# Kernel tuning notes

Hardware: AMD Instinct MI355X
Metric: run time of the kernel (lower is better)

## Reference

```python
import jax, jax.numpy as jnp
import numpy as np

L, H, NH, V, T, B, K = 12, 768, 12, 30522, 512, 4, 21
DH = H // NH
INV_SQRT_DH = 1.0 / float(np.sqrt(DH))
NEG = -1e4  # BERT additive mask value
LN_EPS = 1e-12


def _ln(x, g, b):
    m = x.mean(-1, keepdims=True)
    v = jnp.var(x, axis=-1, keepdims=True)
    return (x - m) * jax.lax.rsqrt(v + LN_EPS) * g + b


def _encoder(input_ids, attention_mask, word_emb, pos_emb, tok_emb, emb_g, emb_b,
             Wqkv, bqkv, Wo, bo, ln1_g, ln1_b, W1, b1, W2, b2, ln2_g, ln2_b):
    Bv, Tv = input_ids.shape
    h = word_emb[input_ids] + pos_emb[None, :Tv] + tok_emb[0]  # token_type_ids = 0
    h = _ln(h, emb_g, emb_b)
    bias = (1.0 - attention_mask[:, None, None, :].astype(h.dtype)) * NEG  # [B,1,1,T]

    def layer(h, xs):
        wqkv, bq, wo, bo_, g1, b1_, w1, bb1, w2, bb2, g2, b2_ = xs
        qkv = h @ wqkv + bq  # [B,T,3H]
        q, k, v = jnp.split(qkv, 3, axis=-1)
        def hd(x):
            return x.reshape(Bv, Tv, NH, DH).transpose(0, 2, 1, 3)
        q, k, v = hd(q), hd(k), hd(v)
        scores = jnp.einsum('bhqd,bhkd->bhqk', q, k) * INV_SQRT_DH + bias
        ctx = jnp.einsum('bhqk,bhkd->bhqd', jax.nn.softmax(scores, axis=-1), v)
        ctx = ctx.transpose(0, 2, 1, 3).reshape(Bv, Tv, H)
        h = _ln(h + ctx @ wo + bo_, g1, b1_)  # post-LN (BERT)
        ff = jax.nn.gelu(h @ w1 + bb1, approximate=False) @ w2 + bb2
        h = _ln(h + ff, g2, b2_)
        return h, None

    h, _ = jax.lax.scan(layer, h, (Wqkv, bqkv, Wo, bo, ln1_g, ln1_b, W1, b1, W2, b2, ln2_g, ln2_b))
    return h


def _crf_nll(emissions, tags, mask, start, end, trans):
    # emissions [B,T,K], tags [B,T] int, mask [B,T] bool; torchcrf reduction='mean'
    Bv, Tv, Kv = emissions.shape
    maskf = mask.astype(emissions.dtype)
    # numerator: score of the gold path
    num = start[tags[:, 0]] + emissions[jnp.arange(Bv), 0, tags[:, 0]]
    em_t = jnp.take_along_axis(emissions, tags[..., None], axis=-1)[..., 0]  # [B,T]
    tr_t = trans[tags[:, :-1], tags[:, 1:]]  # [B,T-1]
    num = num + jnp.sum((tr_t + em_t[:, 1:]) * maskf[:, 1:], axis=1)
    last_idx = mask.sum(axis=1).astype(jnp.int32) - 1
    last_tag = jnp.take_along_axis(tags, last_idx[:, None], axis=1)[:, 0]
    num = num + end[last_tag]
    # denominator: forward algorithm (logsumexp recursion over time)
    alpha0 = start[None, :] + emissions[:, 0]  # [B,K]

    def step(alpha, xs):
        em, m = xs  # em [B,K], m [B] bool
        nxt = jax.scipy.special.logsumexp(alpha[:, :, None] + trans[None] + em[:, None, :], axis=1)
        return jnp.where(m[:, None], nxt, alpha), None

    alpha, _ = jax.lax.scan(step, alpha0, (emissions[:, 1:].transpose(1, 0, 2), mask[:, 1:].T))
    den = jax.scipy.special.logsumexp(alpha + end[None, :], axis=1)
    return -(num - den).mean()


def _viterbi(emissions, mask, start, end, trans):
    # Returns [B,T] int32 best paths; padded tail repeats the last valid tag.
    Bv, Tv, Kv = emissions.shape
    score0 = start[None, :] + emissions[:, 0]
    ident = jnp.broadcast_to(jnp.arange(Kv), (Bv, Kv))

    def step(score, xs):
        em, m = xs
        cand = score[:, :, None] + trans[None]  # [B,K_prev,K_next]
        idx = jnp.where(m[:, None], jnp.argmax(cand, axis=1), ident)
        nxt = jnp.max(cand, axis=1) + em
        return jnp.where(m[:, None], nxt, score), idx

    score, hist = jax.lax.scan(step, score0, (emissions[:, 1:].transpose(1, 0, 2), mask[:, 1:].T))
    last = jnp.argmax(score + end[None, :], axis=1)  # [B]

    def back(nxt_tag, idx):
        prev = jnp.take_along_axis(idx, nxt_tag[:, None], axis=1)[:, 0]
        return prev, nxt_tag

    tag0, rest = jax.lax.scan(back, last, hist, reverse=True)  # rest[i] = tag at t=i+1
    return jnp.concatenate([tag0[None], rest], axis=0).T.astype(jnp.int32)


def setup_inputs():
    key = jax.random.key(0)
    ks = jax.random.split(key, 16)
    s = 0.02

    def n(k, shape):
        return (s * jax.random.normal(k, shape)).astype(jnp.float32)

    def u(k, shape):
        return jax.random.uniform(k, shape, minval=-0.1, maxval=0.1).astype(jnp.float32)

    p = {}
    p['input_ids'] = jax.random.randint(ks[0], (B, T), 0, V)
    lengths = jax.random.randint(ks[1], (B,), T // 2, T + 1)
    p['attention_mask'] = (jnp.arange(T)[None, :] < lengths[:, None]).astype(jnp.int32)
    p['valid_mask'] = p['attention_mask']
    p['labels'] = jax.random.randint(ks[2], (B, T), 0, K)
    p['word_emb'] = n(ks[3], (V, H))
    p['pos_emb'] = n(ks[4], (T, H))
    p['tok_emb'] = n(ks[5], (2, H))
    p['emb_g'] = jnp.ones((H,), jnp.float32)
    p['emb_b'] = jnp.zeros((H,), jnp.float32)
    p['Wqkv'] = n(ks[6], (L, H, 3 * H))
    p['bqkv'] = jnp.zeros((L, 3 * H), jnp.float32)
    p['Wo'] = n(ks[7], (L, H, H))
    p['bo'] = jnp.zeros((L, H), jnp.float32)
    p['ln1_g'] = jnp.ones((L, H), jnp.float32)
    p['ln1_b'] = jnp.zeros((L, H), jnp.float32)
    p['W1'] = n(ks[8], (L, H, 4 * H))
    p['b1'] = jnp.zeros((L, 4 * H), jnp.float32)
    p['W2'] = n(ks[9], (L, 4 * H, H))
    p['b2'] = jnp.zeros((L, H), jnp.float32)
    p['ln2_g'] = jnp.ones((L, H), jnp.float32)
    p['ln2_b'] = jnp.zeros((L, H), jnp.float32)
    p['Wc'] = n(ks[10], (H, K))
    p['bc'] = jnp.zeros((K,), jnp.float32)
    p['crf_start'] = u(ks[11], (K,))
    p['crf_end'] = u(ks[12], (K,))
    p['crf_trans'] = u(ks[13], (K, K))
    return p


def reference(input_ids, attention_mask, valid_mask, labels,
              word_emb, pos_emb, tok_emb, emb_g, emb_b,
              Wqkv, bqkv, Wo, bo, ln1_g, ln1_b, W1, b1, W2, b2, ln2_g, ln2_b,
              Wc, bc, crf_start, crf_end, crf_trans):
    h = _encoder(input_ids, attention_mask, word_emb, pos_emb, tok_emb, emb_g, emb_b,
                 Wqkv, bqkv, Wo, bo, ln1_g, ln1_b, W1, b1, W2, b2, ln2_g, ln2_b)
    emissions = h @ Wc + bc  # dropout is identity in eval/reference mode
    mask = attention_mask.astype(bool)
    nll = _crf_nll(emissions, labels, mask, crf_start, crf_end, crf_trans)
    decoded = _viterbi(emissions, mask, crf_start, crf_end, crf_trans)
    return nll, decoded
```

## Files before the change

kernel.cpp:

```cpp
#include <hip/hip_runtime.h>
#include <math.h>

constexpr int NLAYER = 12;
constexpr int H = 768;
constexpr int NH = 12;
constexpr int DH = 64;
constexpr int T = 512;
constexpr int B = 4;
constexpr int K = 21;
constexpr int BT = B * T;
constexpr float NEGB = -10000.0f;
constexpr float LNEPS = 1e-12f;
constexpr float INV_SQRT_DH = 0.125f;

typedef __attribute__((ext_vector_type(8))) short bf16x8;
typedef __attribute__((ext_vector_type(4))) float f32x4;
typedef __attribute__((ext_vector_type(4))) unsigned short u16x4;

#define WAIT_VMCNT(n) asm volatile("s_waitcnt vmcnt(" #n ")")

__device__ __forceinline__ float wave_sum_f(float v) {
#pragma unroll
  for (int off = 32; off > 0; off >>= 1) v += __shfl_xor(v, off);
  return v;
}
__device__ __forceinline__ int wave_sum_i(int v) {
#pragma unroll
  for (int off = 32; off > 0; off >>= 1) v += __shfl_xor(v, off);
  return v;
}
__device__ __forceinline__ float readlane_f(float v, int i) {
  return __uint_as_float(__builtin_amdgcn_readlane(__float_as_uint(v), i));
}
__device__ __forceinline__ unsigned short f32_bf16_rn(float x) {
  unsigned int u = __float_as_uint(x);
  u += 0x7fffu + ((u >> 16) & 1u);
  return (unsigned short)(u >> 16);
}
__device__ __forceinline__ void split_bf16(float x, unsigned short& h, unsigned short& l) {
  h = f32_bf16_rn(x);
  float hf = __uint_as_float((unsigned int)h << 16);
  l = f32_bf16_rn(x - hf);
}
__device__ __forceinline__ void block_reduce_sum2(float& s, float& q) {
  __shared__ float red[8];
  s = wave_sum_f(s);
  q = wave_sum_f(q);
  int lane = threadIdx.x & 63, wid = threadIdx.x >> 6;
  if (lane == 0) { red[wid] = s; red[4 + wid] = q; }
  __syncthreads();
  s = red[0] + red[1] + red[2] + red[3];
  q = red[4] + red[5] + red[6] + red[7];
}

__global__ __launch_bounds__(256) void embed_ln_kernel(
    const int* __restrict__ ids, const float* __restrict__ wemb,
    const float* __restrict__ pemb, const float* __restrict__ temb,
    const float* __restrict__ g, const float* __restrict__ bta,
    float* __restrict__ h, unsigned short* __restrict__ hh,
    unsigned short* __restrict__ hl) {
  int row = blockIdx.x;
  int t = row % T;
  int id = ids[row];
  const float* wp = wemb + (size_t)id * H;
  const float* pp = pemb + (size_t)t * H;
  float x[3];
  float s = 0.f, q = 0.f;
#pragma unroll
  for (int i = 0; i < 3; i++) {
    int c = threadIdx.x + i * 256;
    x[i] = wp[c] + pp[c] + temb[c];
    s += x[i];
    q += x[i] * x[i];
  }
  block_reduce_sum2(s, q);
  float mean = s * (1.0f / H);
  float var = q * (1.0f / H) - mean * mean;
  float inv = rsqrtf(var + LNEPS);
#pragma unroll
  for (int i = 0; i < 3; i++) {
    int c = threadIdx.x + i * 256;
    float y = (x[i] - mean) * inv * g[c] + bta[c];
    h[(size_t)row * H + c] = y;
    unsigned short yh, yl;
    split_bf16(y, yh, yl);
    hh[(size_t)row * H + c] = yh;
    hl[(size_t)row * H + c] = yl;
  }
}

__global__ __launch_bounds__(256) void add_ln_kernel(
    float* __restrict__ h, const float* __restrict__ add,
    const float* __restrict__ g, const float* __restrict__ bta,
    unsigned short* __restrict__ hh, unsigned short* __restrict__ hl) {
  int row = blockIdx.x;
  size_t base = (size_t)row * H;
  float x[3];
  float s = 0.f, q = 0.f;
#pragma unroll
  for (int i = 0; i < 3; i++) {
    int c = threadIdx.x + i * 256;
    x[i] = h[base + c] + add[base + c];
    s += x[i];
    q += x[i] * x[i];
  }
  block_reduce_sum2(s, q);
  float mean = s * (1.0f / H);
  float var = q * (1.0f / H) - mean * mean;
  float inv = rsqrtf(var + LNEPS);
#pragma unroll
  for (int i = 0; i < 3; i++) {
    int c = threadIdx.x + i * 256;
    float y = (x[i] - mean) * inv * g[c] + bta[c];
    h[base + c] = y;
    unsigned short yh, yl;
    split_bf16(y, yh, yl);
    hh[base + c] = yh;
    hl[base + c] = yl;
  }
}

__global__ __launch_bounds__(256) void wconv_kernel(
    const float* __restrict__ w0, const float* __restrict__ w1,
    const float* __restrict__ w2, const float* __restrict__ w3,
    unsigned short* __restrict__ Wth, unsigned short* __restrict__ Wtl) {
  __shared__ float tile[32][33];
  int bid = blockIdx.x;
  const float* src;
  int Kd, N, tk, tn;
  size_t off;
  if (bid < 1728) {
    src = w0; Kd = 768; N = 2304; tk = bid / 72; tn = bid % 72; off = 0;
  } else if (bid < 2304) {
    int t2 = bid - 1728; src = w1; Kd = 768; N = 768; tk = t2 / 24; tn = t2 % 24;
    off = 1769472;
  } else if (bid < 4608) {
    int t2 = bid - 2304; src = w2; Kd = 768; N = 3072; tk = t2 / 96; tn = t2 % 96;
    off = 2359296;
  } else {
    int t2 = bid - 4608; src = w3; Kd = 3072; N = 768; tk = t2 / 24; tn = t2 % 24;
    off = 4718592;
  }
  int tid = threadIdx.x;
  int k0 = tk * 32, n0 = tn * 32;
  int r = tid >> 3, c = (tid & 7) * 4;
  float4 v = *(const float4*)(src + (size_t)(k0 + r) * N + n0 + c);
  tile[r][c + 0] = v.x; tile[r][c + 1] = v.y; tile[r][c + 2] = v.z; tile[r][c + 3] = v.w;
  __syncthreads();
  u16x4 hv, lv;
#pragma unroll
  for (int q2 = 0; q2 < 4; q2++) {
    unsigned short sh, sl;
    split_bf16(tile[c + q2][r], sh, sl);
    hv[q2] = sh; lv[q2] = sl;
  }
  size_t dst = off + (size_t)(n0 + r) * Kd + k0 + c;
  *(u16x4*)(Wth + dst) = hv;
  *(u16x4*)(Wtl + dst) = lv;
}

template <int OUTMODE>
__global__ __launch_bounds__(256) void gemm_bf3_kernel(
    const unsigned short* __restrict__ Ah, const unsigned short* __restrict__ Al,
    const unsigned short* __restrict__ Wth, const unsigned short* __restrict__ Wtl,
    const float* __restrict__ bias, float* __restrict__ C,
    unsigned short* __restrict__ Ch, unsigned short* __restrict__ Cl,
    unsigned short* __restrict__ Kh, unsigned short* __restrict__ Kl,
    unsigned short* __restrict__ Vth, unsigned short* __restrict__ Vtl,
    int N, int Kd, int ncols) {
  constexpr int AW = 64 * 32;
  constexpr int WW = 128 * 32;
  constexpr int DBS = 2 * AW + 2 * WW;
  __shared__ short lds_s[2 * DBS];
  int tid = threadIdx.x;
  int lane = tid & 63, wid = tid >> 6;
  int wr = wid >> 1, wc = wid & 1;
  int tiles = gridDim.x;
  int q8 = tiles >> 3;
  int wg = (blockIdx.x & 7) * q8 + (blockIdx.x >> 3);
  int bm = (wg / ncols) * 64, bn = (wg % ncols) * 128;

  f32x4 acc[2][4] = {};
  int lrow = lane >> 2;
  int lslot_sw = (lane & 3) ^ ((lrow >> 1) & 3);

  const unsigned short* sbase;
  int rowbase, ldsoff, nchunks;
  if (wid == 0)      { sbase = Ah;  rowbase = bm; ldsoff = 0;            nchunks = 4; }
  else if (wid == 1) { sbase = Al;  rowbase = bm; ldsoff = AW;           nchunks = 4; }
  else if (wid == 2) { sbase = Wth; rowbase = bn; ldsoff = 2 * AW;       nchunks = 8; }
  else               { sbase = Wtl; rowbase = bn; ldsoff = 2 * AW + WW;  nchunks = 8; }

  const unsigned short* srcbase = sbase + (size_t)(rowbase + lrow) * Kd + lslot_sw * 8;

  auto STAGE = [&](int db, int k0) {
#pragma unroll
    for (int c = 0; c < 8; c++) {
      if (c < nchunks) {
        const unsigned short* src = srcbase + (size_t)(c * 16) * Kd + k0;
        char* dst = ((char*)lds_s) + (db * DBS + ldsoff) * 2 + c * 1024 + lane * 16;
        __builtin_amdgcn_global_load_lds(
            (const __attribute__((address_space(1))) void*)src,
            (__attribute__((address_space(3))) void*)dst, 16, 0, 0);
      }
    }
  };

  const int NT = Kd / 32;
  STAGE(0, 0);
  for (int kt = 0; kt < NT; kt++) {
    int cur = kt & 1;
    bool more = (kt + 1 < NT);
    if (more) STAGE(cur ^ 1, (kt + 1) * 32);
    if (more) {
      if (wid < 2) { WAIT_VMCNT(4); } else { WAIT_VMCNT(8); }
    } else {
      WAIT_VMCNT(0);
    }
    __builtin_amdgcn_s_barrier();
    __builtin_amdgcn_sched_barrier(0);

    int lr = lane & 15, lg = lane >> 4;
    int slot = (lg ^ ((lr >> 1) & 3)) * 8;
    int cb = cur * DBS;
    bf16x8 af_h[2], af_l[2], wf_h[4], wf_l[4];
#pragma unroll
    for (int i = 0; i < 2; i++) {
      int e = (wr * 32 + i * 16 + lr) * 32 + slot;
      af_h[i] = *(const bf16x8*)&lds_s[cb + e];
      af_l[i] = *(const bf16x8*)&lds_s[cb + AW + e];
    }
#pragma unroll
    for (int j = 0; j < 4; j++) {
      int e = (wc * 64 + j * 16 + lr) * 32 + slot;
      wf_h[j] = *(const bf16x8*)&lds_s[cb + 2 * AW + e];
      wf_l[j] = *(const bf16x8*)&lds_s[cb + 2 * AW + WW + e];
    }
#pragma unroll
    for (int i = 0; i < 2; i++)
#pragma unroll
      for (int j = 0; j < 4; j++) {
        acc[i][j] = __builtin_amdgcn_mfma_f32_16x16x32_bf16(af_h[i], wf_h[j], acc[i][j], 0, 0, 0);
        acc[i][j] = __builtin_amdgcn_mfma_f32_16x16x32_bf16(af_l[i], wf_h[j], acc[i][j], 0, 0, 0);
        acc[i][j] = __builtin_amdgcn_mfma_f32_16x16x32_bf16(af_h[i], wf_l[j], acc[i][j], 0, 0, 0);
      }
    asm volatile("s_waitcnt lgkmcnt(0)");
    __builtin_amdgcn_sched_barrier(0);
    __builtin_amdgcn_s_barrier();
    __builtin_amdgcn_sched_barrier(0);
  }

  int lr = lane & 15, lg = lane >> 4;
#pragma unroll
  for (int i = 0; i < 2; i++) {
#pragma unroll
    for (int j = 0; j < 4; j++) {
      int row = bm + wr * 32 + i * 16 + lg * 4;
      int col = bn + wc * 64 + j * 16 + lr;
      float bv = bias[col];
      if (OUTMODE == 2) {
        int sec = col / 768;
        int within = col % 768;
        int hidx = within >> 6, d = within & 63;
        int b = row >> 9, t = row & 511;
        int bh = b * NH + hidx;
        if (sec == 2) {
          u16x4 hv, lv;
#pragma unroll
          for (int r = 0; r < 4; r++) {
            unsigned short sh, sl;
            split_bf16(acc[i][j][r] + bv, sh, sl);
            hv[r] = sh; lv[r] = sl;
          }
          size_t idx = ((size_t)bh * 64 + d) * T + t;
          *(u16x4*)(Vth + idx) = hv;
          *(u16x4*)(Vtl + idx) = lv;
        } else {
          unsigned short* dh = (sec == 0) ? Ch : Kh;
          unsigned short* dl = (sec == 0) ? Cl : Kl;
#pragma unroll
          for (int r = 0; r < 4; r++) {
            unsigned short sh, sl;
            split_bf16(acc[i][j][r] + bv, sh, sl);
            size_t idx = ((size_t)bh * T + t + r) * 64 + d;
            dh[idx] = sh;
            dl[idx] = sl;
          }
        }
      } else {
#pragma unroll
        for (int r = 0; r < 4; r++) {
          float v = acc[i][j][r] + bv;
          if (OUTMODE == 1) {
            v = 0.5f * v * (1.0f + erff(v * 0.70710678118654752f));
            unsigned short sh, sl;
            split_bf16(v, sh, sl);
            Ch[(size_t)(row + r) * N + col] = sh;
            Cl[(size_t)(row + r) * N + col] = sl;
          } else {
            C[(size_t)(row + r) * N + col] = v;
          }
        }
      }
    }
  }
}

__global__ __launch_bounds__(256) void attn_kernel(
    const unsigned short* __restrict__ qh, const unsigned short* __restrict__ ql,
    const unsigned short* __restrict__ kh, const unsigned short* __restrict__ kl,
    const unsigned short* __restrict__ vth, const unsigned short* __restrict__ vtl,
    const int* __restrict__ mask,
    unsigned short* __restrict__ cth, unsigned short* __restrict__ ctl) {
  int id = blockIdx.x;
  int bh = (id & 7) * 6 + ((id >> 3) % 6);
  int i0 = (id / 48) * 64;
  int b = bh / NH, hidx = bh % NH;
  int tid = threadIdx.x, lane = tid & 63, w = tid >> 6;
  int lr = lane & 15, lg = lane >> 4;
  __shared__ float bias_s[T];
  __shared__ short p_h[4][16 * 64];
  __shared__ short p_l[4][16 * 64];
  for (int i = tid; i < T; i += 256)
    bias_s[i] = (1.0f - (float)mask[b * T + i]) * NEGB;
  __syncthreads();

  const unsigned short* qb_h = qh + ((size_t)bh * T + i0 + w * 16 + lr) * 64 + lg * 8;
  const unsigned short* qb_l = ql + ((size_t)bh * T + i0 + w * 16 + lr) * 64 + lg * 8;
  bf16x8 qf_h0 = *(const bf16x8*)qb_h;
  bf16x8 qf_h1 = *(const bf16x8*)(qb_h + 32);
  bf16x8 qf_l0 = *(const bf16x8*)qb_l;
  bf16x8 qf_l1 = *(const bf16x8*)(qb_l + 32);

  float m_run[4], l_run[4];
#pragma unroll
  for (int r = 0; r < 4; r++) { m_run[r] = -3.0e38f; l_run[r] = 0.f; }
  f32x4 acc_o[4] = {};

  for (int kt = 0; kt < T / 64; kt++) {
    f32x4 s[4] = {};
#pragma unroll
    for (int jf = 0; jf < 4; jf++) {
      size_t kb = ((size_t)bh * T + kt * 64 + jf * 16 + lr) * 64 + lg * 8;
      bf16x8 kf_h0 = *(const bf16x8*)(kh + kb);
      bf16x8 kf_h1 = *(const bf16x8*)(kh + kb + 32);
      bf16x8 kf_l0 = *(const bf16x8*)(kl + kb);
      bf16x8 kf_l1 = *(const bf16x8*)(kl + kb + 32);
      s[jf] = __builtin_amdgcn_mfma_f32_16x16x32_bf16(qf_h0, kf_h0, s[jf], 0, 0, 0);
      s[jf] = __builtin_amdgcn_mfma_f32_16x16x32_bf16(qf_h1, kf_h1, s[jf], 0, 0, 0);
      s[jf] = __builtin_amdgcn_mfma_f32_16x16x32_bf16(qf_l0, kf_h0, s[jf], 0, 0, 0);
      s[jf] = __builtin_amdgcn_mfma_f32_16x16x32_bf16(qf_l1, kf_h1, s[jf], 0, 0, 0);
      s[jf] = __builtin_amdgcn_mfma_f32_16x16x32_bf16(qf_h0, kf_l0, s[jf], 0, 0, 0);
      s[jf] = __builtin_amdgcn_mfma_f32_16x16x32_bf16(qf_h1, kf_l1, s[jf], 0, 0, 0);
    }
    float mt[4] = {-3.0e38f, -3.0e38f, -3.0e38f, -3.0e38f};
#pragma unroll
    for (int jf = 0; jf < 4; jf++) {
      float bcol = bias_s[kt * 64 + jf * 16 + lr];
#pragma unroll
      for (int r = 0; r < 4; r++) {
        float v = s[jf][r] * INV_SQRT_DH + bcol;
        s[jf][r] = v;
        mt[r] = fmaxf(mt[r], v);
      }
    }
#pragma unroll
    for (int r = 0; r < 4; r++) {
      mt[r] = fmaxf(mt[r], __shfl_xor(mt[r], 1));
      mt[r] = fmaxf(mt[r], __shfl_xor(mt[r], 2));
      mt[r] = fmaxf(mt[r], __shfl_xor(mt[r], 4));
      mt[r] = fmaxf(mt[r], __shfl_xor(mt[r], 8));
    }
#pragma unroll
    for (int r = 0; r < 4; r++) {
      float mn = fmaxf(m_run[r], mt[r]);
      float sc = __expf(m_run[r] - mn);
      m_run[r] = mn;
      l_run[r] *= sc;
#pragma unroll
      for (int jf = 0; jf < 4; jf++) acc_o[jf][r] *= sc;
    }
    float ps[4] = {0.f, 0.f, 0.f, 0.f};
#pragma unroll
    for (int jf = 0; jf < 4; jf++) {
#pragma unroll
      for (int r = 0; r < 4; r++) {
        float p = __expf(s[jf][r] - m_run[r]);
        ps[r] += p;
        unsigned short sh, sl;
        split_bf16(p, sh, sl);
        int q = lg * 4 + r;
        int col = jf * 16 + lr;
        int addr = q * 64 + (((col >> 3) ^ (q & 7)) << 3) + (col & 7);
        p_h[w][addr] = sh;
        p_l[w][addr] = sl;
      }
    }
#pragma unroll
    for (int r = 0; r < 4; r++) {
      ps[r] += __shfl_xor(ps[r], 1);
      ps[r] += __shfl_xor(ps[r], 2);
      ps[r] += __shfl_xor(ps[r], 4);
      ps[r] += __shfl_xor(ps[r], 8);
      l_run[r] += ps[r];
    }
#pragma unroll
    for (int c = 0; c < 2; c++) {
      int aaddr = lr * 64 + (((4 * c + lg) ^ (lr & 7)) << 3);
      bf16x8 pa_h = *(const bf16x8*)&p_h[w][aaddr];
      bf16x8 pa_l = *(const bf16x8*)&p_l[w][aaddr];
#pragma unroll
      for (int jf = 0; jf < 4; jf++) {
        size_t vb = ((size_t)bh * 64 + jf * 16 + lr) * T + kt * 64 + c * 32 + lg * 8;
        bf16x8 vf_h = *(const bf16x8*)(vth + vb);
        bf16x8 vf_l = *(const bf16x8*)(vtl + vb);
        acc_o[jf] = __builtin_amdgcn_mfma_f32_16x16x32_bf16(pa_h, vf_h, acc_o[jf], 0, 0, 0);
        acc_o[jf] = __builtin_amdgcn_mfma_f32_16x16x32_bf16(pa_l, vf_h, acc_o[jf], 0, 0, 0);
        acc_o[jf] = __builtin_amdgcn_mfma_f32_16x16x32_bf16(pa_h, vf_l, acc_o[jf], 0, 0, 0);
      }
    }
  }
  float inv[4];
#pragma unroll
  for (int r = 0; r < 4; r++) inv[r] = 1.0f / l_run[r];
#pragma unroll
  for (int jf = 0; jf < 4; jf++) {
#pragma unroll
    for (int r = 0; r < 4; r++) {
      float v = acc_o[jf][r] * inv[r];
      unsigned short sh, sl;
      split_bf16(v, sh, sl);
      size_t idx = ((size_t)(b * T) + i0 + w * 16 + lg * 4 + r) * H + hidx * 64 + jf * 16 + lr;
      cth[idx] = sh;
      ctl[idx] = sl;
    }
  }
}

__global__ __launch_bounds__(256) void wct_kernel(
    const float* __restrict__ Wc, float* __restrict__ WcT) {
  int id = blockIdx.x * 256 + threadIdx.x;
  int k = id / H, d = id % H;
  WcT[id] = Wc[d * K + k];
}

__global__ __launch_bounds__(256) void classifier_kernel(
    const float* __restrict__ h, const float* __restrict__ WcT,
    const float* __restrict__ bc, float* __restrict__ em) {
  int id = blockIdx.x * 256 + threadIdx.x;
  if (id >= BT * K) return;
  int row = id / K, k = id % K;
  const float4* h4 = (const float4*)(h + (size_t)row * H);
  const float4* w4 = (const float4*)(WcT + (size_t)k * H);
  float acc = bc[k];
  for (int d = 0; d < H / 4; d++) {
    float4 a = h4[d], b = w4[d];
    acc = fmaf(a.x, b.x, acc);
    acc = fmaf(a.y, b.y, acc);
    acc = fmaf(a.z, b.z, acc);
    acc = fmaf(a.w, b.w, acc);
  }
  em[id] = acc;
}

#define MRG(vo, io, va, ia, vb, ib) \
  float vo = ((vb) > (va)) ? (vb) : (va); \
  int io = ((vb) > (va)) ? (ib) : (ia);

__global__ __launch_bounds__(64) void crf_fused_kernel(
    const float* __restrict__ em, const int* __restrict__ labels,
    const int* __restrict__ mask, const float* __restrict__ start,
    const float* __restrict__ endv, const float* __restrict__ trans,
    float* __restrict__ parts, float* __restrict__ outdec) {
  __shared__ float em_s[T * K];
  __shared__ int mask_s[T];
  __shared__ unsigned char hist_s[(T - 1) * K];
  __shared__ float sc_s[32];
  int b = blockIdx.x & 3;
  int role = blockIdx.x >> 2;
  int j = threadIdx.x;
  const float* eb = em + (size_t)b * T * K;
  for (int i = j; i < T * K / 4; i += 64)
    ((float4*)em_s)[i] = ((const float4*)eb)[i];
  for (int i = j; i < T; i += 64) mask_s[i] = mask[b * T + i];
  __syncthreads();
  bool act = (j < K);
  float tr[K];
#pragma unroll
  for (int i = 0; i < K; i++) tr[i] = act ? trans[i * K + j] : 0.f;

  int cntloc = 0;
  for (int t = j; t < T; t += 64) cntloc += mask_s[t];
  int cnt = wave_sum_i(cntloc);

  if (role == 0) {
    const int* tb = labels + b * T;
    float numloc = 0.f;
    for (int t = j; t < T; t += 64) {
      if (t >= 1 && mask_s[t]) {
        int tp = tb[t - 1], tc = tb[t];
        numloc += trans[tp * K + tc] + em_s[t * K + tc];
      }
    }
    float num = wave_sum_f(numloc);
    float etr[K];
#pragma unroll
    for (int i = 0; i < K; i++) etr[i] = __expf(tr[i]);
    float alpha = act ? (start[j] + em_s[j]) : 0.f;
    float emv = act ? em_s[K + j] : 0.f;
    for (int t = 1; t < cnt; t++) {
      float emv_n = (act && (t + 1) < cnt) ? em_s[(t + 1) * K + j] : 0.f;
      float m0 = readlane_f(alpha, 0);
      float ee = __expf(alpha - m0);
      float e0 = readlane_f(ee, 0),  e1 = readlane_f(ee, 1),  e2 = readlane_f(ee, 2);
      float e3 = readlane_f(ee, 3),  e4 = readlane_f(ee, 4),  e5 = readlane_f(ee, 5);
      float e6 = readlane_f(ee, 6),  e7 = readlane_f(ee, 7),  e8 = readlane_f(ee, 8);
      float e9 = readlane_f(ee, 9),  e10 = readlane_f(ee, 10), e11 = readlane_f(ee, 11);
      float e12 = readlane_f(ee, 12), e13 = readlane_f(ee, 13), e14 = readlane_f(ee, 14);
      float e15 = readlane_f(ee, 15), e16 = readlane_f(ee, 16), e17 = readlane_f(ee, 17);
      float e18 = readlane_f(ee, 18), e19 = readlane_f(ee, 19), e20 = readlane_f(ee, 20);
      float a0 = fmaf(e16, etr[16], fmaf(e12, etr[12], fmaf(e8, etr[8],  fmaf(e4, etr[4], e0 * etr[0]))));
      float a1 = fmaf(e17, etr[17], fmaf(e13, etr[13], fmaf(e9, etr[9],  fmaf(e5, etr[5], e1 * etr[1]))));
      float a2 = fmaf(e18, etr[18], fmaf(e14, etr[14], fmaf(e10, etr[10], fmaf(e6, etr[6], e2 * etr[2]))));
      float a3 = fmaf(e19, etr[19], fmaf(e15, etr[15], fmaf(e11, etr[11], fmaf(e7, etr[7], e3 * etr[3]))));
      float ssum = fmaf(e20, etr[20], (a0 + a1) + (a2 + a3));
      float nxt = __logf(ssum) + m0 + emv;
      if (act) alpha = nxt;
      emv = emv_n;
    }
    float aj = act ? (alpha + endv[j]) : -3.0e38f;
    float mm = aj;
#pragma unroll
    for (int off = 32; off > 0; off >>= 1) mm = fmaxf(mm, __shfl_xor(mm, off));
    float e2v = act ? __expf(aj - mm) : 0.f;
    float s2 = wave_sum_f(e2v);
    float den = __logf(s2) + mm;
    if (j == 0) {
      int tag0 = tb[0];
      float numtot = num + start[tag0] + em_s[tag0] + endv[tb[cnt - 1]];
      parts[b] = numtot - den;
    }
  } else {
    float score = act ? (start[j] + em_s[j]) : 0.f;
    float emv = act ? em_s[K + j] : 0.f;
    for (int t = 1; t < cnt; t++) {
      float emv_n = (act && (t + 1) < cnt) ? em_s[(t + 1) * K + j] : 0.f;
      float c0 = readlane_f(score, 0) + tr[0],   c1 = readlane_f(score, 1) + tr[1];
      float c2 = readlane_f(score, 2) + tr[2],   c3 = readlane_f(score, 3) + tr[3];
      float c4 = readlane_f(score, 4) + tr[4],   c5 = readlane_f(score, 5) + tr[5];
      float c6 = readlane_f(score, 6) + tr[6],   c7 = readlane_f(score, 7) + tr[7];
      float c8 = readlane_f(score, 8) + tr[8],   c9 = readlane_f(score, 9) + tr[9];
      float c10 = readlane_f(score, 10) + tr[10], c11 = readlane_f(score, 11) + tr[11];
      float c12 = readlane_f(score, 12) + tr[12], c13 = readlane_f(score, 13) + tr[13];
      float c14 = readlane_f(score, 14) + tr[14], c15 = readlane_f(score, 15) + tr[15];
      float c16 = readlane_f(score, 16) + tr[16], c17 = readlane_f(score, 17) + tr[17];
      float c18 = readlane_f(score, 18) + tr[18], c19 = readlane_f(score, 19) + tr[19];
      float c20 = readlane_f(score, 20) + tr[20];
      MRG(m0v, m0i, c0, 0, c1, 1)
      MRG(m1v, m1i, c2, 2, c3, 3)
      MRG(m2v, m2i, c4, 4, c5, 5)
      MRG(m3v, m3i, c6, 6, c7, 7)
      MRG(m4v, m4i, c8, 8, c9, 9)
      MRG(m5v, m5i, c10, 10, c11, 11)
      MRG(m6v, m6i, c12, 12, c13, 13)
      MRG(m7v, m7i, c14, 14, c15, 15)
      MRG(m8v, m8i, c16, 16, c17, 17)
      MRG(m9v, m9i, c18, 18, c19, 19)
      MRG(p0v, p0i, m0v, m0i, m1v, m1i)
      MRG(p1v, p1i, m2v, m2i, m3v, m3i)
      MRG(p2v, p2i, m4v, m4i, m5v, m5i)
      MRG(p3v, p3i, m6v, m6i, m7v, m7i)
      MRG(p4v, p4i, m8v, m8i, m9v, m9i)
      MRG(r0v, r0i, p0v, p0i, p1v, p1i)
      MRG(r1v, r1i, p2v, p2i, p3v, p3i)
      MRG(r2v, r2i, p4v, p4i, c20, 20)
      MRG(s0v, s0i, r0v, r0i, r1v, r1i)
      MRG(fv, fi, s0v, s0i, r2v, r2i)
      if (act) {
        hist_s[(t - 1) * K + j] = (unsigned char)fi;
        score = fv + emv;
      }
      emv = emv_n;
    }
    if (act) sc_s[j] = score + endv[j];
    __syncthreads();
    if (j == 0) {
      float best = -3.0e38f;
      int last = 0;
#pragma unroll
      for (int i = 0; i < K; i++)
        if (sc_s[i] > best) { best = sc_s[i]; last = i; }
      for (int t = cnt - 1; t < T; t++) outdec[b * T + t] = (float)last;
      int cur = last;
      for (int t = cnt - 1; t >= 1; t--) {
        cur = hist_s[(t - 1) * K + cur];
        outdec[b * T + (t - 1)] = (float)cur;
      }
    }
  }
}

__global__ void nll_final_kernel(const float* __restrict__ parts,
                                 float* __restrict__ out) {
  out[0] = -0.25f * (parts[0] + parts[1] + parts[2] + parts[3]);
}

extern "C" void kernel_launch(void* const* d_in, const int* in_sizes, int n_in,
                              void* d_out, int out_size, void* d_ws, size_t ws_size,
                              hipStream_t stream) {
  (void)in_sizes; (void)n_in; (void)out_size; (void)ws_size;
  const int* ids    = (const int*)d_in[0];
  const int* amask  = (const int*)d_in[1];
  const int* labels = (const int*)d_in[3];
  const float* wemb = (const float*)d_in[4];
  const float* pemb = (const float*)d_in[5];
  const float* temb = (const float*)d_in[6];
  const float* eg   = (const float*)d_in[7];
  const float* ebta = (const float*)d_in[8];
  const float* Wqkv = (const float*)d_in[9];
  const float* bqkv = (const float*)d_in[10];
  const float* Wo   = (const float*)d_in[11];
  const float* bo   = (const float*)d_in[12];
  const float* ln1g = (const float*)d_in[13];
  const float* ln1b = (const float*)d_in[14];
  const float* W1   = (const float*)d_in[15];
  const float* b1   = (const float*)d_in[16];
  const float* W2   = (const float*)d_in[17];
  const float* b2   = (const float*)d_in[18];
  const float* ln2g = (const float*)d_in[19];
  const float* ln2b = (const float*)d_in[20];
  const float* Wc   = (const float*)d_in[21];
  const float* bc   = (const float*)d_in[22];
  const float* cst  = (const float*)d_in[23];
  const float* cen  = (const float*)d_in[24];
  const float* ctr  = (const float*)d_in[25];
  float* out = (float*)d_out;

  float* ws = (float*)d_ws;
  float* fp = ws;
  float* h = fp;                 fp += 1572864;
  unsigned short* hh  = (unsigned short*)fp; fp += 786432;
  unsigned short* hl  = (unsigned short*)fp; fp += 786432;
  unsigned short* qhp = (unsigned short*)fp; fp += 786432;
  unsigned short* qlp = (unsigned short*)fp; fp += 786432;
  unsigned short* khp = (unsigned short*)fp; fp += 786432;
  unsigned short* klp = (unsigned short*)fp; fp += 786432;
  unsigned short* vtp = (unsigned short*)fp; fp += 786432;
  unsigned short* vlp = (unsigned short*)fp; fp += 786432;
  unsigned short* cth = (unsigned short*)fp; fp += 786432;
  unsigned short* ctl = (unsigned short*)fp; fp += 786432;
  float* tmp = fp;               fp += 1572864;
  unsigned short* gh  = (unsigned short*)fp; fp += 3145728;
  unsigned short* gl  = (unsigned short*)fp; fp += 3145728;
  unsigned short* Wth = (unsigned short*)fp; fp += 3538944;
  unsigned short* Wtl = (unsigned short*)fp; fp += 3538944;
  float* em = fp;                fp += 43008;
  float* parts = fp;             fp += 8;
  float* WcT = fp;               fp += 16128;

  embed_ln_kernel<<<BT, 256, 0, stream>>>(ids, wemb, pemb, temb, eg, ebta, h, hh, hl);
  wct_kernel<<<63, 256, 0, stream>>>(Wc, WcT);

  for (int l = 0; l < NLAYER; l++) {
    const float* bqkv_l = bqkv + (size_t)l * 3 * H;
    const float* bo_l   = bo + (size_t)l * H;
    const float* b1_l   = b1 + (size_t)l * 4 * H;
    const float* b2_l   = b2 + (size_t)l * H;

    wconv_kernel<<<6912, 256, 0, stream>>>(
        Wqkv + (size_t)l * H * 3 * H, Wo + (size_t)l * H * H,
        W1 + (size_t)l * H * 4 * H, W2 + (size_t)l * 4 * H * H, Wth, Wtl);

    gemm_bf3_kernel<2><<<576, 256, 0, stream>>>(
        hh, hl, Wth, Wtl, bqkv_l, nullptr, qhp, qlp, khp, klp,
        vtp, vlp, 3 * H, H, 18);
    attn_kernel<<<384, 256, 0, stream>>>(
        qhp, qlp, khp, klp, vtp, vlp, amask, cth, ctl);
    gemm_bf3_kernel<0><<<192, 256, 0, stream>>>(
        cth, ctl, Wth + 1769472, Wtl + 1769472, bo_l, tmp,
        nullptr, nullptr, nullptr, nullptr, nullptr, nullptr, H, H, 6);
    add_ln_kernel<<<BT, 256, 0, stream>>>(h, tmp, ln1g + (size_t)l * H, ln1b + (size_t)l * H, hh, hl);
    gemm_bf3_kernel<1><<<768, 256, 0, stream>>>(
        hh, hl, Wth + 2359296, Wtl + 2359296, b1_l, nullptr, gh, gl,
        nullptr, nullptr, nullptr, nullptr, 4 * H, H, 24);
    gemm_bf3_kernel<0><<<192, 256, 0, stream>>>(
        gh, gl, Wth + 4718592, Wtl + 4718592, b2_l, tmp,
        nullptr, nullptr, nullptr, nullptr, nullptr, nullptr, H, 4 * H, 6);
    add_ln_kernel<<<BT, 256, 0, stream>>>(h, tmp, ln2g + (size_t)l * H, ln2b + (size_t)l * H, hh, hl);
  }

  classifier_kernel<<<(BT * K + 255) / 256, 256, 0, stream>>>(h, WcT, bc, em);
  crf_fused_kernel<<<8, 64, 0, stream>>>(em, labels, amask, cst, cen, ctr, parts, out + 1);
  nll_final_kernel<<<1, 1, 0, stream>>>(parts, out);
}
```

Measured before the change: 3.153 ms.

## Overlap next-layer weight conversion with attention; load GEMM operands directly into registers

Weight split/transpose for layer l+1 is now fused into the attention launch as extra blocks, writing into a double-buffered weight area so conversion overlaps attention instead of running as its own serial kernel. Layer 0 weights are converted once up front. The GEMM also drops its LDS double-buffered staging and instead loads MFMA fragments straight from global memory into registers, with a two-stage register ping-pong. This removes LDS traffic and barriers but gives up cross-wave operand sharing through LDS, relies on L1/L2 for reuse, and increases register pressure.

```diff
diff --git a/kernel.cpp b/kernel.cpp
--- a/kernel.cpp
+++ b/kernel.cpp
@@ -17,7 +17,7 @@
 typedef __attribute__((ext_vector_type(4))) float f32x4;
 typedef __attribute__((ext_vector_type(4))) unsigned short u16x4;
 
-#define WAIT_VMCNT(n) asm volatile("s_waitcnt vmcnt(" #n ")")
+constexpr size_t WL_SHORTS = 7077888;
 
 __device__ __forceinline__ float wave_sum_f(float v) {
 #pragma unroll
@@ -120,12 +120,11 @@
   }
 }
 
-__global__ __launch_bounds__(256) void wconv_kernel(
-    const float* __restrict__ w0, const float* __restrict__ w1,
+__device__ __forceinline__ void wconv_body(
+    int bid, int tid, const float* __restrict__ w0, const float* __restrict__ w1,
     const float* __restrict__ w2, const float* __restrict__ w3,
-    unsigned short* __restrict__ Wth, unsigned short* __restrict__ Wtl) {
-  __shared__ float tile[32][33];
-  int bid = blockIdx.x;
+    unsigned short* __restrict__ Wth, unsigned short* __restrict__ Wtl,
+    float (*tile)[33]) {
   const float* src;
   int Kd, N, tk, tn;
   size_t off;
@@ -141,7 +140,6 @@
     int t2 = bid - 4608; src = w3; Kd = 3072; N = 768; tk = t2 / 24; tn = t2 % 24;
     off = 4718592;
   }
-  int tid = threadIdx.x;
   int k0 = tk * 32, n0 = tn * 32;
   int r = tid >> 3, c = (tid & 7) * 4;
   float4 v = *(const float4*)(src + (size_t)(k0 + r) * N + n0 + c);
@@ -159,8 +157,42 @@
   *(u16x4*)(Wtl + dst) = lv;
 }
 
+__global__ __launch_bounds__(256) void wconv_kernel(
+    const float* __restrict__ w0, const float* __restrict__ w1,
+    const float* __restrict__ w2, const float* __restrict__ w3,
+    unsigned short* __restrict__ Wth, unsigned short* __restrict__ Wtl) {
+  __shared__ float tile[32][33];
+  wconv_body(blockIdx.x, threadIdx.x, w0, w1, w2, w3, Wth, Wtl, tile);
+}
+
+#define MFMA3(AI, AJ, AH, AL, WH, WL)                                              \
+  acc[AI][AJ] = __builtin_amdgcn_mfma_f32_16x16x32_bf16(AH, WH, acc[AI][AJ], 0, 0, 0); \
+  acc[AI][AJ] = __builtin_amdgcn_mfma_f32_16x16x32_bf16(AL, WH, acc[AI][AJ], 0, 0, 0); \
+  acc[AI][AJ] = __builtin_amdgcn_mfma_f32_16x16x32_bf16(AH, WL, acc[AI][AJ], 0, 0, 0);
+
+#define DECLS(S) bf16x8 a0h##S, a1h##S, a0l##S, a1l##S,                 \
+      w0h##S, w1h##S, w2h##S, w3h##S, w0l##S, w1l##S, w2l##S, w3l##S
+
+#define LOADS(S, KT) do { int ko = (KT) * 32;                            \
+    a0h##S = *(const bf16x8*)(aH0 + ko); a1h##S = *(const bf16x8*)(aH1 + ko); \
+    a0l##S = *(const bf16x8*)(aL0 + ko); a1l##S = *(const bf16x8*)(aL1 + ko); \
+    w0h##S = *(const bf16x8*)(wH0 + ko); w1h##S = *(const bf16x8*)(wH1 + ko); \
+    w2h##S = *(const bf16x8*)(wH2 + ko); w3h##S = *(const bf16x8*)(wH3 + ko); \
+    w0l##S = *(const bf16x8*)(wL0 + ko); w1l##S = *(const bf16x8*)(wL1 + ko); \
+    w2l##S = *(const bf16x8*)(wL2 + ko); w3l##S = *(const bf16x8*)(wL3 + ko); } while (0)
+
+#define MFMAS(S)                                        \
+  MFMA3(0, 0, a0h##S, a0l##S, w0h##S, w0l##S)           \
+  MFMA3(0, 1, a0h##S, a0l##S, w1h##S, w1l##S)           \
+  MFMA3(0, 2, a0h##S, a0l##S, w2h##S, w2l##S)           \
+  MFMA3(0, 3, a0h##S, a0l##S, w3h##S, w3l##S)           \
+  MFMA3(1, 0, a1h##S, a1l##S, w0h##S, w0l##S)           \
+  MFMA3(1, 1, a1h##S, a1l##S, w1h##S, w1l##S)           \
+  MFMA3(1, 2, a1h##S, a1l##S, w2h##S, w2l##S)           \
+  MFMA3(1, 3, a1h##S, a1l##S, w3h##S, w3l##S)
+
 template <int OUTMODE>
-__global__ __launch_bounds__(256) void gemm_bf3_kernel(
+__global__ __launch_bounds__(256) void gemm_reg_kernel(
     const unsigned short* __restrict__ Ah, const unsigned short* __restrict__ Al,
     const unsigned short* __restrict__ Wth, const unsigned short* __restrict__ Wtl,
     const float* __restrict__ bias, float* __restrict__ C,
@@ -168,10 +200,6 @@
     unsigned short* __restrict__ Kh, unsigned short* __restrict__ Kl,
     unsigned short* __restrict__ Vth, unsigned short* __restrict__ Vtl,
     int N, int Kd, int ncols) {
-  constexpr int AW = 64 * 32;
-  constexpr int WW = 128 * 32;
-  constexpr int DBS = 2 * AW + 2 * WW;
-  __shared__ short lds_s[2 * DBS];
   int tid = threadIdx.x;
   int lane = tid & 63, wid = tid >> 6;
   int wr = wid >> 1, wc = wid & 1;
@@ -179,78 +207,33 @@
   int q8 = tiles >> 3;
   int wg = (blockIdx.x & 7) * q8 + (blockIdx.x >> 3);
   int bm = (wg / ncols) * 64, bn = (wg % ncols) * 128;
+  int lr = lane & 15, lg = lane >> 4;
+
+  const unsigned short* aH0 = Ah + (size_t)(bm + wr * 32 + lr) * Kd + lg * 8;
+  const unsigned short* aH1 = aH0 + (size_t)16 * Kd;
+  const unsigned short* aL0 = Al + (size_t)(bm + wr * 32 + lr) * Kd + lg * 8;
+  const unsigned short* aL1 = aL0 + (size_t)16 * Kd;
+  const unsigned short* wH0 = Wth + (size_t)(bn + wc * 64 + lr) * Kd + lg * 8;
+  const unsigned short* wH1 = wH0 + (size_t)16 * Kd;
+  const unsigned short* wH2 = wH0 + (size_t)32 * Kd;
+  const unsigned short* wH3 = wH0 + (size_t)48 * Kd;
+  const unsigned short* wL0 = Wtl + (size_t)(bn + wc * 64 + lr) * Kd + lg * 8;
+  const unsigned short* wL1 = wL0 + (size_t)16 * Kd;
+  const unsigned short* wL2 = wL0 + (size_t)32 * Kd;
+  const unsigned short* wL3 = wL0 + (size_t)48 * Kd;
 
   f32x4 acc[2][4] = {};
-  int lrow = lane >> 2;
-  int lslot_sw = (lane & 3) ^ ((lrow >> 1) & 3);
-
-  const unsigned short* sbase;
-  int rowbase, ldsoff, nchunks;
-  if (wid == 0)      { sbase = Ah;  rowbase = bm; ldsoff = 0;            nchunks = 4; }
-  else if (wid == 1) { sbase = Al;  rowbase = bm; ldsoff = AW;           nchunks = 4; }
-  else if (wid == 2) { sbase = Wth; rowbase = bn; ldsoff = 2 * AW;       nchunks = 8; }
-  else               { sbase = Wtl; rowbase = bn; ldsoff = 2 * AW + WW;  nchunks = 8; }
-
-  const unsigned short* srcbase = sbase + (size_t)(rowbase + lrow) * Kd + lslot_sw * 8;
-
-  auto STAGE = [&](int db, int k0) {
-#pragma unroll
-    for (int c = 0; c < 8; c++) {
-      if (c < nchunks) {
-        const unsigned short* src = srcbase + (size_t)(c * 16) * Kd + k0;
-        char* dst = ((char*)lds_s) + (db * DBS + ldsoff) * 2 + c * 1024 + lane * 16;
-        __builtin_amdgcn_global_load_lds(
-            (const __attribute__((address_space(1))) void*)src,
-            (__attribute__((address_space(3))) void*)dst, 16, 0, 0);
-      }
-    }
-  };
-
+  DECLS(A);
+  DECLS(Bv);
   const int NT = Kd / 32;
-  STAGE(0, 0);
-  for (int kt = 0; kt < NT; kt++) {
-    int cur = kt & 1;
-    bool more = (kt + 1 < NT);
-    if (more) STAGE(cur ^ 1, (kt + 1) * 32);
-    if (more) {
-      if (wid < 2) { WAIT_VMCNT(4); } else { WAIT_VMCNT(8); }
-    } else {
-      WAIT_VMCNT(0);
-    }
-    __builtin_amdgcn_s_barrier();
-    __builtin_amdgcn_sched_barrier(0);
-
-    int lr = lane & 15, lg = lane >> 4;
-    int slot = (lg ^ ((lr >> 1) & 3)) * 8;
-    int cb = cur * DBS;
-    bf16x8 af_h[2], af_l[2], wf_h[4], wf_l[4];
-#pragma unroll
-    for (int i = 0; i < 2; i++) {
-      int e = (wr * 32 + i * 16 + lr) * 32 + slot;
-      af_h[i] = *(const bf16x8*)&lds_s[cb + e];
-      af_l[i] = *(const bf16x8*)&lds_s[cb + AW + e];
-    }
-#pragma unroll
-    for (int j = 0; j < 4; j++) {
-      int e = (wc * 64 + j * 16 + lr) * 32 + slot;
-      wf_h[j] = *(const bf16x8*)&lds_s[cb + 2 * AW + e];
-      wf_l[j] = *(const bf16x8*)&lds_s[cb + 2 * AW + WW + e];
-    }
-#pragma unroll
-    for (int i = 0; i < 2; i++)
-#pragma unroll
-      for (int j = 0; j < 4; j++) {
-        acc[i][j] = __builtin_amdgcn_mfma_f32_16x16x32_bf16(af_h[i], wf_h[j], acc[i][j], 0, 0, 0);
-        acc[i][j] = __builtin_amdgcn_mfma_f32_16x16x32_bf16(af_l[i], wf_h[j], acc[i][j], 0, 0, 0);
-        acc[i][j] = __builtin_amdgcn_mfma_f32_16x16x32_bf16(af_h[i], wf_l[j], acc[i][j], 0, 0, 0);
-      }
-    asm volatile("s_waitcnt lgkmcnt(0)");
-    __builtin_amdgcn_sched_barrier(0);
-    __builtin_amdgcn_s_barrier();
-    __builtin_amdgcn_sched_barrier(0);
-  }
-
-  int lr = lane & 15, lg = lane >> 4;
+  LOADS(A, 0);
+  for (int kt = 0; kt < NT; kt += 2) {
+    LOADS(Bv, kt + 1);
+    MFMAS(A);
+    if (kt + 2 < NT) LOADS(A, kt + 2);
+    MFMAS(Bv);
+  }
+
 #pragma unroll
   for (int i = 0; i < 2; i++) {
 #pragma unroll
@@ -306,21 +289,32 @@
   }
 }
 
-__global__ __launch_bounds__(256) void attn_kernel(
+__global__ __launch_bounds__(256) void attn_wconv_kernel(
     const unsigned short* __restrict__ qh, const unsigned short* __restrict__ ql,
     const unsigned short* __restrict__ kh, const unsigned short* __restrict__ kl,
     const unsigned short* __restrict__ vth, const unsigned short* __restrict__ vtl,
     const int* __restrict__ mask,
-    unsigned short* __restrict__ cth, unsigned short* __restrict__ ctl) {
+    unsigned short* __restrict__ cth, unsigned short* __restrict__ ctl,
+    const float* __restrict__ nw0, const float* __restrict__ nw1,
+    const float* __restrict__ nw2, const float* __restrict__ nw3,
+    unsigned short* __restrict__ nWth, unsigned short* __restrict__ nWtl) {
+  __shared__ float bias_s[T];
+  __shared__ short p_h[4][16 * 64];
+  __shared__ short p_l[4][16 * 64];
+  int tid = threadIdx.x;
+
+  if (blockIdx.x >= 384) {
+    float (*tile)[33] = (float(*)[33]) & p_h[0][0];
+    wconv_body(blockIdx.x - 384, tid, nw0, nw1, nw2, nw3, nWth, nWtl, tile);
+    return;
+  }
+
   int id = blockIdx.x;
   int bh = (id & 7) * 6 + ((id >> 3) % 6);
   int i0 = (id / 48) * 64;
   int b = bh / NH, hidx = bh % NH;
-  int tid = threadIdx.x, lane = tid & 63, w = tid >> 6;
+  int lane = tid & 63, w = tid >> 6;
   int lr = lane & 15, lg = lane >> 4;
-  __shared__ float bias_s[T];
-  __shared__ short p_h[4][16 * 64];
-  __shared__ short p_l[4][16 * 64];
   for (int i = tid; i < T; i += 256)
     bias_s[i] = (1.0f - (float)mask[b * T + i]) * NEGB;
   __syncthreads();
@@ -652,38 +646,45 @@
   float* tmp = fp;               fp += 1572864;
   unsigned short* gh  = (unsigned short*)fp; fp += 3145728;
   unsigned short* gl  = (unsigned short*)fp; fp += 3145728;
-  unsigned short* Wth = (unsigned short*)fp; fp += 3538944;
-  unsigned short* Wtl = (unsigned short*)fp; fp += 3538944;
   float* em = fp;                fp += 43008;
   float* parts = fp;             fp += 8;
   float* WcT = fp;               fp += 16128;
+  unsigned short* wb0h = (unsigned short*)fp; fp += 3538944;
+  unsigned short* wb0l = (unsigned short*)fp; fp += 3538944;
+  unsigned short* wb1h = (unsigned short*)fp; fp += 3538944;
+  unsigned short* wb1l = (unsigned short*)fp; fp += 3538944;
 
   embed_ln_kernel<<<BT, 256, 0, stream>>>(ids, wemb, pemb, temb, eg, ebta, h, hh, hl);
   wct_kernel<<<63, 256, 0, stream>>>(Wc, WcT);
+  wconv_kernel<<<6912, 256, 0, stream>>>(Wqkv, Wo, W1, W2, wb0h, wb0l);
 
   for (int l = 0; l < NLAYER; l++) {
     const float* bqkv_l = bqkv + (size_t)l * 3 * H;
     const float* bo_l   = bo + (size_t)l * H;
     const float* b1_l   = b1 + (size_t)l * 4 * H;
     const float* b2_l   = b2 + (size_t)l * H;
-
-    wconv_kernel<<<6912, 256, 0, stream>>>(
-        Wqkv + (size_t)l * H * 3 * H, Wo + (size_t)l * H * H,
-        W1 + (size_t)l * H * 4 * H, W2 + (size_t)l * 4 * H * H, Wth, Wtl);
-
-    gemm_bf3_kernel<2><<<576, 256, 0, stream>>>(
+    unsigned short* Wth = (l & 1) ? wb1h : wb0h;
+    unsigned short* Wtl = (l & 1) ? wb1l : wb0l;
+    unsigned short* nWth = (l & 1) ? wb0h : wb1h;
+    unsigned short* nWtl = (l & 1) ? wb0l : wb1l;
+    int ln = (l + 1 < NLAYER) ? l + 1 : l;
+
+    gemm_reg_kernel<2><<<576, 256, 0, stream>>>(
         hh, hl, Wth, Wtl, bqkv_l, nullptr, qhp, qlp, khp, klp,
         vtp, vlp, 3 * H, H, 18);
-    attn_kernel<<<384, 256, 0, stream>>>(
-        qhp, qlp, khp, klp, vtp, vlp, amask, cth, ctl);
-    gemm_bf3_kernel<0><<<192, 256, 0, stream>>>(
+    int agrid = (l + 1 < NLAYER) ? (384 + 6912) : 384;
+    attn_wconv_kernel<<<agrid, 256, 0, stream>>>(
+        qhp, qlp, khp, klp, vtp, vlp, amask, cth, ctl,
+        Wqkv + (size_t)ln * H * 3 * H, Wo + (size_t)ln * H * H,
+        W1 + (size_t)ln * H * 4 * H, W2 + (size_t)ln * 4 * H * H, nWth, nWtl);
+    gemm_reg_kernel<0><<<192, 256, 0, stream>>>(
         cth, ctl, Wth + 1769472, Wtl + 1769472, bo_l, tmp,
         nullptr, nullptr, nullptr, nullptr, nullptr, nullptr, H, H, 6);
     add_ln_kernel<<<BT, 256, 0, stream>>>(h, tmp, ln1g + (size_t)l * H, ln1b + (size_t)l * H, hh, hl);
-    gemm_bf3_kernel<1><<<768, 256, 0, stream>>>(
+    gemm_reg_kernel<1><<<768, 256, 0, stream>>>(
         hh, hl, Wth + 2359296, Wtl + 2359296, b1_l, nullptr, gh, gl,
         nullptr, nullptr, nullptr, nullptr, 4 * H, H, 24);
-    gemm_bf3_kernel<0><<<192, 256, 0, stream>>>(
+    gemm_reg_kernel<0><<<192, 256, 0, stream>>>(
         gh, gl, Wth + 4718592, Wtl + 4718592, b2_l, tmp,
         nullptr, nullptr, nullptr, nullptr, nullptr, nullptr, H, 4 * H, 6);
     add_ln_kernel<<<BT, 256, 0, stream>>>(h, tmp, ln2g + (size_t)l * H, ln2b + (size_t)l * H, hh, hl);
```

Result: slower. 5.863 ms (+85.9%).

## Double-buffer weight conversion and overlap next layer's conversion with attention

Applied to the files above, without the earlier changes.

Converts the next layer's weights into a second bf16 hi/lo buffer using extra blocks appended to the attention kernel's grid, so the conversion shares GPU time with attention instead of running as its own launch. Only layer 0's conversion stays a standalone kernel. The aim is to hide the per-layer conversion cost and launch overhead and to fill idle CUs, since attention uses only 384 blocks. It costs a second weight buffer, and it puts attention and conversion blocks in one kernel with shared LDS, so attention blocks may be slowed by the bandwidth the conversion uses.

```diff
diff --git a/kernel.cpp b/kernel.cpp
--- a/kernel.cpp
+++ b/kernel.cpp
@@ -120,12 +120,11 @@
   }
 }
 
-__global__ __launch_bounds__(256) void wconv_kernel(
-    const float* __restrict__ w0, const float* __restrict__ w1,
+__device__ __forceinline__ void wconv_body(
+    int bid, int tid, const float* __restrict__ w0, const float* __restrict__ w1,
     const float* __restrict__ w2, const float* __restrict__ w3,
-    unsigned short* __restrict__ Wth, unsigned short* __restrict__ Wtl) {
-  __shared__ float tile[32][33];
-  int bid = blockIdx.x;
+    unsigned short* __restrict__ Wth, unsigned short* __restrict__ Wtl,
+    float (*tile)[33]) {
   const float* src;
   int Kd, N, tk, tn;
   size_t off;
@@ -141,7 +140,6 @@
     int t2 = bid - 4608; src = w3; Kd = 3072; N = 768; tk = t2 / 24; tn = t2 % 24;
     off = 4718592;
   }
-  int tid = threadIdx.x;
   int k0 = tk * 32, n0 = tn * 32;
   int r = tid >> 3, c = (tid & 7) * 4;
   float4 v = *(const float4*)(src + (size_t)(k0 + r) * N + n0 + c);
@@ -157,6 +155,14 @@
   size_t dst = off + (size_t)(n0 + r) * Kd + k0 + c;
   *(u16x4*)(Wth + dst) = hv;
   *(u16x4*)(Wtl + dst) = lv;
+}
+
+__global__ __launch_bounds__(256) void wconv_kernel(
+    const float* __restrict__ w0, const float* __restrict__ w1,
+    const float* __restrict__ w2, const float* __restrict__ w3,
+    unsigned short* __restrict__ Wth, unsigned short* __restrict__ Wtl) {
+  __shared__ float tile[32][33];
+  wconv_body(blockIdx.x, threadIdx.x, w0, w1, w2, w3, Wth, Wtl, tile);
 }
 
 template <int OUTMODE>
@@ -306,21 +312,32 @@
   }
 }
 
-__global__ __launch_bounds__(256) void attn_kernel(
+__global__ __launch_bounds__(256) void attn_wconv_kernel(
     const unsigned short* __restrict__ qh, const unsigned short* __restrict__ ql,
     const unsigned short* __restrict__ kh, const unsigned short* __restrict__ kl,
     const unsigned short* __restrict__ vth, const unsigned short* __restrict__ vtl,
     const int* __restrict__ mask,
-    unsigned short* __restrict__ cth, unsigned short* __restrict__ ctl) {
+    unsigned short* __restrict__ cth, unsigned short* __restrict__ ctl,
+    const float* __restrict__ nw0, const float* __restrict__ nw1,
+    const float* __restrict__ nw2, const float* __restrict__ nw3,
+    unsigned short* __restrict__ nWth, unsigned short* __restrict__ nWtl) {
+  __shared__ float bias_s[T];
+  __shared__ short p_h[4][16 * 64];
+  __shared__ short p_l[4][16 * 64];
+  int tid = threadIdx.x;
+
+  if (blockIdx.x >= 384) {
+    float (*tile)[33] = (float(*)[33]) & p_h[0][0];
+    wconv_body(blockIdx.x - 384, tid, nw0, nw1, nw2, nw3, nWth, nWtl, tile);
+    return;
+  }
+
   int id = blockIdx.x;
   int bh = (id & 7) * 6 + ((id >> 3) % 6);
   int i0 = (id / 48) * 64;
   int b = bh / NH, hidx = bh % NH;
-  int tid = threadIdx.x, lane = tid & 63, w = tid >> 6;
+  int lane = tid & 63, w = tid >> 6;
   int lr = lane & 15, lg = lane >> 4;
-  __shared__ float bias_s[T];
-  __shared__ short p_h[4][16 * 64];
-  __shared__ short p_l[4][16 * 64];
   for (int i = tid; i < T; i += 256)
     bias_s[i] = (1.0f - (float)mask[b * T + i]) * NEGB;
   __syncthreads();
@@ -652,30 +669,37 @@
   float* tmp = fp;               fp += 1572864;
   unsigned short* gh  = (unsigned short*)fp; fp += 3145728;
   unsigned short* gl  = (unsigned short*)fp; fp += 3145728;
-  unsigned short* Wth = (unsigned short*)fp; fp += 3538944;
-  unsigned short* Wtl = (unsigned short*)fp; fp += 3538944;
   float* em = fp;                fp += 43008;
   float* parts = fp;             fp += 8;
   float* WcT = fp;               fp += 16128;
+  unsigned short* wb0h = (unsigned short*)fp; fp += 3538944;
+  unsigned short* wb0l = (unsigned short*)fp; fp += 3538944;
+  unsigned short* wb1h = (unsigned short*)fp; fp += 3538944;
+  unsigned short* wb1l = (unsigned short*)fp; fp += 3538944;
 
   embed_ln_kernel<<<BT, 256, 0, stream>>>(ids, wemb, pemb, temb, eg, ebta, h, hh, hl);
   wct_kernel<<<63, 256, 0, stream>>>(Wc, WcT);
+  wconv_kernel<<<6912, 256, 0, stream>>>(Wqkv, Wo, W1, W2, wb0h, wb0l);
 
   for (int l = 0; l < NLAYER; l++) {
     const float* bqkv_l = bqkv + (size_t)l * 3 * H;
     const float* bo_l   = bo + (size_t)l * H;
     const float* b1_l   = b1 + (size_t)l * 4 * H;
     const float* b2_l   = b2 + (size_t)l * H;
-
-    wconv_kernel<<<6912, 256, 0, stream>>>(
-        Wqkv + (size_t)l * H * 3 * H, Wo + (size_t)l * H * H,
-        W1 + (size_t)l * H * 4 * H, W2 + (size_t)l * 4 * H * H, Wth, Wtl);
+    unsigned short* Wth = (l & 1) ? wb1h : wb0h;
+    unsigned short* Wtl = (l & 1) ? wb1l : wb0l;
+    unsigned short* nWth = (l & 1) ? wb0h : wb1h;
+    unsigned short* nWtl = (l & 1) ? wb0l : wb1l;
+    int ln = (l + 1 < NLAYER) ? l + 1 : l;
 
     gemm_bf3_kernel<2><<<576, 256, 0, stream>>>(
         hh, hl, Wth, Wtl, bqkv_l, nullptr, qhp, qlp, khp, klp,
         vtp, vlp, 3 * H, H, 18);
-    attn_kernel<<<384, 256, 0, stream>>>(
-        qhp, qlp, khp, klp, vtp, vlp, amask, cth, ctl);
+    int agrid = (l + 1 < NLAYER) ? (384 + 6912) : 384;
+    attn_wconv_kernel<<<agrid, 256, 0, stream>>>(
+        qhp, qlp, khp, klp, vtp, vlp, amask, cth, ctl,
+        Wqkv + (size_t)ln * H * 3 * H, Wo + (size_t)ln * H * H,
+        W1 + (size_t)ln * H * 4 * H, W2 + (size_t)ln * 4 * H * H, nWth, nWtl);
     gemm_bf3_kernel<0><<<192, 256, 0, stream>>>(
         cth, ctl, Wth + 1769472, Wtl + 1769472, bo_l, tmp,
         nullptr, nullptr, nullptr, nullptr, nullptr, nullptr, H, H, 6);
```

Result: slower. 3.477 ms (+10.3%).
